# Kernel tuning notes

Hardware: AMD Instinct MI355X
Metric: run time of the kernel (lower is better)

The kernel has to match this reference:

```python
import jax, jax.numpy as jnp
import numpy as np

N = 500_000      # evaluation points
M = 8            # Nmode
K = 4            # Clebsch branches
NPSI = 256       # psi grid points
X0 = 0.0
H = 1.0 / (NPSI - 1)


def _cubic_interp(f, x):
    """Cubic Hermite spline (C1, FD slopes) on a uniform psi grid, extrapolating.
    f: [NPSI, C] table, x: [N] query points -> [N, C]."""
    u = (x - X0) / H
    i = jnp.clip(jnp.floor(u).astype(jnp.int32), 0, NPSI - 2)
    s = (u - i.astype(x.dtype))[:, None]           # local coord, may be outside [0,1] (extrap)
    d = jnp.gradient(f, axis=0) / H                # FD derivatives [NPSI, C]
    f0, f1, d0, d1 = f[i], f[i + 1], d[i], d[i + 1]
    s2 = s * s
    s3 = s2 * s
    return ((2 * s3 - 3 * s2 + 1) * f0 + (s3 - 2 * s2 + s) * H * d0
            + (-2 * s3 + 3 * s2) * f1 + (s3 - s2) * H * d1)


def setup_inputs() -> dict:
    key = jax.random.key(0)
    ks = jax.random.split(key, 12)
    pg = jnp.linspace(0.0, 1.0, NPSI, dtype=jnp.float32)
    inp = {
        "t": jnp.float32(0.5),
        "psi": jax.random.uniform(ks[0], (N,), jnp.float32, 0.05, 0.95),
        "theta": jax.random.uniform(ks[1], (N,), jnp.float32, -jnp.pi, jnp.pi),
        "varphi": jax.random.uniform(ks[2], (N,), jnp.float32, 0.0, 2 * jnp.pi),
        # smooth Clebsch profiles on the psi grid (safety factor q and alpha offset)
        "q_vals": (1.0 + 2.5 * pg ** 2).astype(jnp.float32),
        "aoff_vals": (0.3 * jnp.sin(2 * jnp.pi * pg)).astype(jnp.float32),
        "theta0": jax.random.uniform(ks[3], (M,), jnp.float32, -jnp.pi, jnp.pi),
        "omega": jax.random.uniform(ks[4], (M,), jnp.float32, 0.5, 2.0),
        "psi0": jax.random.uniform(ks[5], (M,), jnp.float32, 0.2, 0.8),
        "psi_scale": jax.random.uniform(ks[6], (M,), jnp.float32, 0.05, 0.15),
        "alpha_scale": jax.random.uniform(ks[7], (M,), jnp.float32, 0.2, 0.6),
        "gh_coefs": 0.5 * jax.random.normal(ks[8], (M, 4, 6), jnp.float32),
        "n": jax.random.randint(ks[9], (M,), 1, 12, jnp.int32),
    }
    return inp


def reference(t, psi, theta, varphi, q_vals, aoff_vals, theta0, omega, psi0,
              psi_scale, alpha_scale, gh_coefs, n):
    # Clebsch mapping: alpha_k(psi, theta) = q(psi) * (theta + 2*pi*k) + alpha_off(psi)
    qa = _cubic_interp(jnp.stack([q_vals, aoff_vals], axis=-1), psi)  # [N,2]
    q, aoff = qa[:, 0], qa[:, 1]
    kk = 2 * jnp.pi * jnp.arange(K, dtype=psi.dtype)
    alpha = q[:, None] * (theta[:, None] + kk[None, :]) + aoff[:, None]    # [N,K]
    # alpha0(psi; mode) table built from the Clebsch profiles (mirrors __init__)
    alpha0_grid = q_vals[:, None] * theta0[None, :] + aoff_vals[:, None]   # [NPSI,M]
    alpha0 = _cubic_interp(alpha0_grid, psi)                               # [N,M]

    x = (psi[:, None] - psi0) / psi_scale                                  # [N,M]
    y = (alpha[:, None, :] - alpha0[:, :, None]) / alpha_scale[None, :, None]  # [N,M,K]
    g = jnp.exp(-0.5 * (x[:, :, None] ** 2 + y ** 2))                      # [N,M,K]

    c = gh_coefs  # [M,4,6]
    h10 = x[:, :, None, None]
    h01 = y[:, :, :, None]
    h20 = (4 * x ** 2 - 2)[:, :, None, None]
    h11 = (x[:, :, None] * y)[:, :, :, None]
    h02 = (4 * y ** 2 - 2)[:, :, :, None]
    p = (c[None, :, None, :, 0] + c[None, :, None, :, 1] * h10
         + c[None, :, None, :, 2] * h01 + c[None, :, None, :, 3] * h20
         + c[None, :, None, :, 4] * h11 + c[None, :, None, :, 5] * h02)    # [N,M,K,4]
    p = p * g[:, :, :, None]

    nf = n.astype(psi.dtype)
    # alpha - alpha0 == y * alpha_scale
    phase = omega[None, :, None] * t - nf[None, :, None] * (
        varphi[:, None, None] - y * alpha_scale[None, :, None])            # [N,M,K]
    cp, sp = jnp.cos(phase), jnp.sin(phase)
    phi = jnp.sum(p[..., 0] * cp - p[..., 1] * sp, axis=(1, 2))            # [N]
    apar = jnp.sum(p[..., 2] * cp - p[..., 3] * sp, axis=(1, 2))           # [N]
    return phi, apar
```

## Files before the change

### kernel.cpp

```cpp
#include <hip/hip_runtime.h>

#define NPSI 256
#define MM 8
#define KK 4

#if __has_builtin(__builtin_amdgcn_exp2f)
#define EXP2F(x) __builtin_amdgcn_exp2f(x)
#else
#define EXP2F(x) exp2f(x)
#endif

#define SIN_REV(x) __builtin_amdgcn_sinf(x)
#define COS_REV(x) __builtin_amdgcn_cosf(x)

__global__ __launch_bounds__(256) void eik_kernel(
    const float* __restrict__ t_ptr,
    const float* __restrict__ psi_a,
    const float* __restrict__ theta_a,
    const float* __restrict__ varphi_a,
    const float* __restrict__ q_vals,
    const float* __restrict__ theta0_a,
    const float* __restrict__ omega_a,
    const float* __restrict__ psi0_a,
    const float* __restrict__ psi_scale_a,
    const float* __restrict__ alpha_scale_a,
    const float* __restrict__ gh_a,
    const int*   __restrict__ n_a,
    float* __restrict__ out,
    int N)
{
    int idx = blockIdx.x * blockDim.x + threadIdx.x;
    if (idx >= N) return;

    const float INV2PI = 0.15915494309189533577f;
    const float TWO_PI = 6.28318530717958647692f;
    const float NEXPC  = -0.72134752044448170368f;

    const float t      = t_ptr[0];
    const float psi    = psi_a[idx];
    const float theta  = theta_a[idx];
    const float varphi = varphi_a[idx];

    float u = psi * (float)(NPSI - 1);
    int   i = (int)floorf(u);
    i = min(max(i, 0), NPSI - 2);
    float s  = u - (float)i;
    float f0 = q_vals[i];
    float f1 = q_vals[i + 1];
    float d0 = (i == 0)        ? (f1 - f0) : 0.5f * (f1 - q_vals[i - 1]);
    float d1 = (i == NPSI - 2) ? (f1 - f0) : 0.5f * (q_vals[i + 2] - f0);
    float s2 = s * s, s3 = s2 * s;
    float q  = (2.f * s3 - 3.f * s2 + 1.f) * f0
             + (s3 - 2.f * s2 + s)         * d0
             + (-2.f * s3 + 3.f * s2)      * f1
             + (s3 - s2)                   * d1;


    const float q2pi = q * TWO_PI;
    const float tt   = t * INV2PI;
    const float v2p  = varphi * INV2PI;

    float phi = 0.f, apar = 0.f;

    #pragma unroll 2
    for (int m = 0; m < MM; ++m) {
        const float theta0 = theta0_a[m];
        const float omega  = omega_a[m];
        const float psi0   = psi0_a[m];
        const float inv_ps = __builtin_amdgcn_rcpf(psi_scale_a[m]);
        const float inv_as = __builtin_amdgcn_rcpf(alpha_scale_a[m]);
        const float nf     = (float)n_a[m];
        const float* c     = gh_a + m * 24;

        const float x  = (psi - psi0) * inv_ps;
        const float x2 = x * x;
        const float x4 = 4.f * x2;

        float pa[4], pb[4], pf[4];
        #pragma unroll
        for (int comp = 0; comp < 4; ++comp) {
            const float c0 = c[comp*6+0], c1 = c[comp*6+1], c2 = c[comp*6+2];
            const float c3 = c[comp*6+3], c4 = c[comp*6+4], c5 = c[comp*6+5];
            const float ssum = c3 + c5;
            const float a0   = fmaf(-2.f, ssum, c0);
            pa[comp] = fmaf(c3, x4, fmaf(c1, x, a0));
            pb[comp] = fmaf(c4, x, c2);
            pf[comp] = c5;
        }

        const float dth    = theta - theta0;
        const float qdth   = q * dth;
        const float y0     = qdth * inv_as;
        const float dy     = q2pi * inv_as;
        const float dphrev = nf * q;
        const float base    = fmaf(omega, tt, -nf * v2p);
        const float p0rev   = fmaf(nf, qdth * INV2PI, base);

        #pragma unroll
        for (int k = 0; k < KK; ++k) {
            const float kf = (float)k;
            const float y  = fmaf(kf, dy, y0);
            const float ph = fmaf(kf, dphrev, p0rev);
            const float sp = SIN_REV(ph);
            const float cp = COS_REV(ph);
            const float t2 = fmaf(y, y, x2);
            const float y4 = fmaf(4.f, t2, -x4);
            const float g  = EXP2F(t2 * NEXPC);
            const float gc = g * cp;
            const float gs = g * sp;
            const float p0 = fmaf(pf[0], y4, fmaf(pb[0], y, pa[0]));
            const float p1 = fmaf(pf[1], y4, fmaf(pb[1], y, pa[1]));
            const float p2 = fmaf(pf[2], y4, fmaf(pb[2], y, pa[2]));
            const float p3 = fmaf(pf[3], y4, fmaf(pb[3], y, pa[3]));
            phi  = fmaf(p0, gc, phi);
            phi  = fmaf(-p1, gs, phi);
            apar = fmaf(p2, gc, apar);
            apar = fmaf(-p3, gs, apar);
        }
    }

    out[idx]     = phi;
    out[idx + N] = apar;
}

extern "C" void kernel_launch(void* const* d_in, const int* in_sizes, int n_in,
                              void* d_out, int out_size, void* d_ws, size_t ws_size,
                              hipStream_t stream) {
    const float* t       = (const float*)d_in[0];
    const float* psi     = (const float*)d_in[1];
    const float* theta   = (const float*)d_in[2];
    const float* varphi  = (const float*)d_in[3];
    const float* q_vals  = (const float*)d_in[4];
    const float* theta0  = (const float*)d_in[6];
    const float* omega   = (const float*)d_in[7];
    const float* psi0    = (const float*)d_in[8];
    const float* psc     = (const float*)d_in[9];
    const float* asc     = (const float*)d_in[10];
    const float* gh      = (const float*)d_in[11];
    const int*   n_arr   = (const int*)d_in[12];

    const int N = in_sizes[1];
    float* out = (float*)d_out;

    const int block = 256;
    const int grid  = (N + block - 1) / block;
    eik_kernel<<<grid, block, 0, stream>>>(t, psi, theta, varphi, q_vals,
                                           theta0, omega, psi0, psc, asc,
                                           gh, n_arr, out, N);
}
```

Before: 96.16 us.

## Process two points per thread with packed FMA and sin/cos angle-addition recurrence

```diff
diff --git a/kernel.cpp b/kernel.cpp
--- a/kernel.cpp
+++ b/kernel.cpp
@@ -4,14 +4,33 @@
 #define MM 8
 #define KK 4
 
+typedef float v2f __attribute__((ext_vector_type(2)));
+
 #if __has_builtin(__builtin_amdgcn_exp2f)
 #define EXP2F(x) __builtin_amdgcn_exp2f(x)
 #else
 #define EXP2F(x) exp2f(x)
 #endif
-
 #define SIN_REV(x) __builtin_amdgcn_sinf(x)
 #define COS_REV(x) __builtin_amdgcn_cosf(x)
+
+#define VFMA(a,b,c) __builtin_elementwise_fma((v2f)(a),(v2f)(b),(v2f)(c))
+
+__device__ inline float cubic_q(const float* __restrict__ q_vals, float psi) {
+    float u = psi * (float)(NPSI - 1);
+    int   i = (int)floorf(u);
+    i = min(max(i, 0), NPSI - 2);
+    float s  = u - (float)i;
+    float f0 = q_vals[i];
+    float f1 = q_vals[i + 1];
+    float d0 = (i == 0)        ? (f1 - f0) : 0.5f * (f1 - q_vals[i - 1]);
+    float d1 = (i == NPSI - 2) ? (f1 - f0) : 0.5f * (q_vals[i + 2] - f0);
+    float s2 = s * s, s3 = s2 * s;
+    return (2.f * s3 - 3.f * s2 + 1.f) * f0
+         + (s3 - 2.f * s2 + s)         * d0
+         + (-2.f * s3 + 3.f * s2)      * f1
+         + (s3 - s2)                   * d1;
+}
 
 __global__ __launch_bounds__(256) void eik_kernel(
     const float* __restrict__ t_ptr,
@@ -29,40 +48,39 @@
     float* __restrict__ out,
     int N)
 {
-    int idx = blockIdx.x * blockDim.x + threadIdx.x;
-    if (idx >= N) return;
+    const int gid   = blockIdx.x * blockDim.x + threadIdx.x;
+    const int i0    = 2 * gid;
+    if (i0 >= N) return;
+    const bool full = (i0 + 1 < N);
 
     const float INV2PI = 0.15915494309189533577f;
     const float TWO_PI = 6.28318530717958647692f;
     const float NEXPC  = -0.72134752044448170368f;
 
-    const float t      = t_ptr[0];
-    const float psi    = psi_a[idx];
-    const float theta  = theta_a[idx];
-    const float varphi = varphi_a[idx];
+    const float t = t_ptr[0];
 
-    float u = psi * (float)(NPSI - 1);
-    int   i = (int)floorf(u);
-    i = min(max(i, 0), NPSI - 2);
-    float s  = u - (float)i;
-    float f0 = q_vals[i];
-    float f1 = q_vals[i + 1];
-    float d0 = (i == 0)        ? (f1 - f0) : 0.5f * (f1 - q_vals[i - 1]);
-    float d1 = (i == NPSI - 2) ? (f1 - f0) : 0.5f * (q_vals[i + 2] - f0);
-    float s2 = s * s, s3 = s2 * s;
-    float q  = (2.f * s3 - 3.f * s2 + 1.f) * f0
-             + (s3 - 2.f * s2 + s)         * d0
-             + (-2.f * s3 + 3.f * s2)      * f1
-             + (s3 - s2)                   * d1;
+    v2f psi, theta, varphi;
+    if (full) {
+        psi    = ((const v2f*)psi_a)[gid];
+        theta  = ((const v2f*)theta_a)[gid];
+        varphi = ((const v2f*)varphi_a)[gid];
+    } else {
+        psi.x = psi.y = psi_a[i0];
+        theta.x = theta.y = theta_a[i0];
+        varphi.x = varphi.y = varphi_a[i0];
+    }
 
+    v2f q;
+    q.x = cubic_q(q_vals, psi.x);
+    q.y = cubic_q(q_vals, psi.y);
 
-    const float q2pi = q * TWO_PI;
-    const float tt   = t * INV2PI;
-    const float v2p  = varphi * INV2PI;
+    const v2f q2pi = q * TWO_PI;
+    const float tt = t * INV2PI;
+    const v2f  v2p = varphi * INV2PI;
 
-    float phi = 0.f, apar = 0.f;
+    v2f phi = (v2f)0.f, apar = (v2f)0.f;
 
-    #pragma unroll 2
+    #pragma unroll 1
     for (int m = 0; m < MM; ++m) {
         const float theta0 = theta0_a[m];
         const float omega  = omega_a[m];
@@ -72,55 +90,70 @@
         const float nf     = (float)n_a[m];
         const float* c     = gh_a + m * 24;
 
-        const float x  = (psi - psi0) * inv_ps;
-        const float x2 = x * x;
-        const float x4 = 4.f * x2;
+        const v2f x  = (psi - psi0) * inv_ps;
+        const v2f x2 = x * x;
+        const v2f x4 = 4.f * x2;
 
-        float pa[4], pb[4], pf[4];
+        v2f pa[4], pb[4];
+        float pf[4];
         #pragma unroll
         for (int comp = 0; comp < 4; ++comp) {
             const float c0 = c[comp*6+0], c1 = c[comp*6+1], c2 = c[comp*6+2];
             const float c3 = c[comp*6+3], c4 = c[comp*6+4], c5 = c[comp*6+5];
-            const float ssum = c3 + c5;
-            const float a0   = fmaf(-2.f, ssum, c0);
-            pa[comp] = fmaf(c3, x4, fmaf(c1, x, a0));
-            pb[comp] = fmaf(c4, x, c2);
+            const float a0 = fmaf(-2.f, c3 + c5, c0);
+            pa[comp] = VFMA((v2f)c3, x4, VFMA((v2f)c1, x, (v2f)a0));
+            pb[comp] = VFMA((v2f)c4, x, (v2f)c2);
             pf[comp] = c5;
         }
 
-        const float dth    = theta - theta0;
-        const float qdth   = q * dth;
-        const float y0     = qdth * inv_as;
-        const float dy     = q2pi * inv_as;
-        const float dphrev = nf * q;
-        const float base    = fmaf(omega, tt, -nf * v2p);
-        const float p0rev   = fmaf(nf, qdth * INV2PI, base);
+        const v2f dth  = theta - theta0;
+        const v2f qdth = q * dth;
+        v2f y          = qdth * inv_as;
+        const v2f dy   = q2pi * inv_as;
+        const v2f dphr = nf * q;
+        const v2f p0r  = VFMA((v2f)nf, qdth * INV2PI,
+                              VFMA((v2f)omega, (v2f)tt, -nf * v2p));
+
+        v2f cp, sp, cd, sd;
+        cp.x = COS_REV(p0r.x);  cp.y = COS_REV(p0r.y);
+        sp.x = SIN_REV(p0r.x);  sp.y = SIN_REV(p0r.y);
+        cd.x = COS_REV(dphr.x); cd.y = COS_REV(dphr.y);
+        sd.x = SIN_REV(dphr.x); sd.y = SIN_REV(dphr.y);
 
         #pragma unroll
         for (int k = 0; k < KK; ++k) {
-            const float kf = (float)k;
-            const float y  = fmaf(kf, dy, y0);
-            const float ph = fmaf(kf, dphrev, p0rev);
-            const float sp = SIN_REV(ph);
-            const float cp = COS_REV(ph);
-            const float t2 = fmaf(y, y, x2);
-            const float y4 = fmaf(4.f, t2, -x4);
-            const float g  = EXP2F(t2 * NEXPC);
-            const float gc = g * cp;
-            const float gs = g * sp;
-            const float p0 = fmaf(pf[0], y4, fmaf(pb[0], y, pa[0]));
-            const float p1 = fmaf(pf[1], y4, fmaf(pb[1], y, pa[1]));
-            const float p2 = fmaf(pf[2], y4, fmaf(pb[2], y, pa[2]));
-            const float p3 = fmaf(pf[3], y4, fmaf(pb[3], y, pa[3]));
-            phi  = fmaf(p0, gc, phi);
-            phi  = fmaf(-p1, gs, phi);
-            apar = fmaf(p2, gc, apar);
-            apar = fmaf(-p3, gs, apar);
+            const v2f t2 = VFMA(y, y, x2);
+            const v2f y4 = VFMA((v2f)4.f, t2, -x4);
+            const v2f ta = t2 * NEXPC;
+            v2f g;
+            g.x = EXP2F(ta.x);
+            g.y = EXP2F(ta.y);
+            const v2f gc = g * cp;
+            const v2f gs = g * sp;
+            const v2f p0 = VFMA((v2f)pf[0], y4, VFMA(pb[0], y, pa[0]));
+            const v2f p1 = VFMA((v2f)pf[1], y4, VFMA(pb[1], y, pa[1]));
+            const v2f p2 = VFMA((v2f)pf[2], y4, VFMA(pb[2], y, pa[2]));
+            const v2f p3 = VFMA((v2f)pf[3], y4, VFMA(pb[3], y, pa[3]));
+            phi  = VFMA(p0, gc, phi);
+            phi  = VFMA(-p1, gs, phi);
+            apar = VFMA(p2, gc, apar);
+            apar = VFMA(-p3, gs, apar);
+            if (k < KK - 1) {
+                const v2f ncp = VFMA(cp, cd, -(sp * sd));
+                const v2f nsp = VFMA(sp, cd,  cp * sd);
+                cp = ncp; sp = nsp;
+                y = y + dy;
+            }
         }
     }
 
-    out[idx]     = phi;
-    out[idx + N] = apar;
+    if (full) {
+        *(v2f*)(out + i0)     = phi;
+        *(v2f*)(out + N + i0) = apar;
+    } else {
+        out[i0]     = phi.x;
+        out[N + i0] = apar.x;
+    }
 }
 
 extern "C" void kernel_launch(void* const* d_in, const int* in_sizes, int n_in,
@@ -142,8 +175,9 @@
     const int N = in_sizes[1];
     float* out = (float*)d_out;
 
+    const int npair = (N + 1) / 2;
     const int block = 256;
-    const int grid  = (N + block - 1) / block;
+    const int grid  = (npair + block - 1) / block;
     eik_kernel<<<grid, block, 0, stream>>>(t, psi, theta, varphi, q_vals,
                                            theta0, omega, psi0, psc, asc,
                                            gh, n_arr, out, N);
```

New measurement: 92.99 us (median of 2 runs). 1.03x faster.
